# Kernel optimization log

Measured on AMD Instinct MI355X. Metric: run time of the kernel, lower is better.

The kernel has to match this reference:

```python
import jax, jax.numpy as jnp
import numpy as np

B, N, F_IN, F_OUT = 64, 1024, 200, 200
NEG_SLOPE = 0.2  # PyG GATConv default


def setup_inputs() -> dict:
    key = jax.random.key(0)
    k1, k2, k3, k4, k5 = jax.random.split(key, 5)
    return {
        "x": jax.random.normal(k1, (B, 1, N, F_IN), dtype=jnp.float32),
        "W": jax.random.normal(k2, (F_IN, F_OUT), dtype=jnp.float32) * 0.05,
        "att_src": jax.random.normal(k3, (F_OUT,), dtype=jnp.float32) * 0.05,
        "att_dst": jax.random.normal(k4, (F_OUT,), dtype=jnp.float32) * 0.05,
        "bias": jax.random.normal(k5, (F_OUT,), dtype=jnp.float32) * 0.05,
    }


def reference(x, W, att_src, att_dst, bias):
    # x: [B, 1, N, F_IN]; module flattens to (B*N) nodes but the edge_index
    # only spans node ids 0..N-1 (complete graph minus self loops). PyG's
    # GATConv re-adds self loops for ALL B*N nodes, so:
    #   nodes 0..N-1 : dense softmax attention over all N nodes (incl. self)
    #   nodes >= N   : only the self loop -> out = h_i + bias
    b, _, n, f = x.shape
    xf = x.reshape(b * n, f)
    h = xf @ W                                # [B*N, F_OUT] linear transform

    h0 = h[:n]                                # first graph's nodes
    a_s = h0 @ att_src                        # [N] per-source score
    a_d = h0 @ att_dst                        # [N] per-target score
    # score[i, j] = leaky_relu(a_dst[i] + a_src[j]), softmax over sources j
    scores = jax.nn.leaky_relu(a_d[:, None] + a_s[None, :], negative_slope=NEG_SLOPE)
    alpha = jax.nn.softmax(scores, axis=1)    # [N, N]
    out0 = alpha @ h0 + bias                  # [N, F_OUT]

    out_rest = h[n:] + bias                   # self-loop only -> alpha == 1
    out = jnp.concatenate([out0, out_rest], axis=0)
    return out.reshape(b, n, -1)[:, None]     # [B, 1, N, F_OUT]
```

## Files before the change

kernel.cpp:

```cpp
#include <hip/hip_runtime.h>

#define BATCH 64
#define NNODE 1024
#define FDIM  200
#define MROWS (BATCH * NNODE)
#define NEG_SLOPE 0.2f

#define NKT 7
#define NNT 13

typedef short s16x8 __attribute__((ext_vector_type(8)));
typedef float f32x4 __attribute__((ext_vector_type(4)));


__device__ __forceinline__ unsigned int f2bf(float f) {
    unsigned int u = __float_as_uint(f);
    return (u + 0x7fffu + ((u >> 16) & 1u)) >> 16;
}
__device__ __forceinline__ unsigned int pack2(float a, float b) {
    return f2bf(a) | (f2bf(b) << 16);
}

__global__ __launch_bounds__(64) void k_prep(const float* __restrict__ W,
                                             const float* __restrict__ att_src,
                                             const float* __restrict__ att_dst,
                                             unsigned short* __restrict__ fragW,
                                             float* __restrict__ wsv,
                                             float* __restrict__ wdv)
{
    const int b    = blockIdx.x;
    const int lane = threadIdx.x;

    if (b < 91) {
        const int kt   = b / NNT;
        const int nt   = b - kt * NNT;
        const int n    = nt * 16 + (lane & 15);
        const int kb   = kt * 32 + (lane >> 4) * 8;
        s16x8 v;
        #pragma unroll
        for (int j = 0; j < 8; ++j) {
            int k = kb + j;
            float f = (k < FDIM && n < FDIM) ? W[k * FDIM + n] : 0.f;
            v[j] = (short)f2bf(f);
        }
        ((s16x8*)(fragW + (size_t)b * 512))[lane] = v;
    } else {
        const int kk = b - 91;
        const float* Wr = W + kk * FDIM;
        float ps = 0.f, pd = 0.f;
        #pragma unroll
        for (int i = 0; i < 4; ++i) {
            int n = lane + i * 64;
            if (n < FDIM) {
                float wv = Wr[n];
                ps = fmaf(wv, att_src[n], ps);
                pd = fmaf(wv, att_dst[n], pd);
            }
        }
        #pragma unroll
        for (int off = 32; off; off >>= 1) {
            ps += __shfl_down(ps, off);
            pd += __shfl_down(pd, off);
        }
        if (lane == 0) { wsv[kk] = ps; wdv[kk] = pd; }
    }
}

__global__ __launch_bounds__(256) void k_av(const float* __restrict__ x,
                                            const float* __restrict__ wsv,
                                            const float* __restrict__ wdv,
                                            float* __restrict__ a_s,
                                            float* __restrict__ a_d)
{
    const int tid  = threadIdx.x;
    const int lane = tid & 63;
    const int row  = blockIdx.x * 4 + (tid >> 6);
    const float* xr = x + (size_t)row * FDIM;
    float ss = 0.f, sd = 0.f;
    for (int k = lane; k < FDIM; k += 64) {
        float xv = xr[k];
        ss = fmaf(xv, wsv[k], ss);
        sd = fmaf(xv, wdv[k], sd);
    }
    #pragma unroll
    for (int off = 32; off; off >>= 1) {
        ss += __shfl_down(ss, off);
        sd += __shfl_down(sd, off);
    }
    if (lane == 0) { a_s[row] = ss; a_d[row] = sd; }
}

__global__ __launch_bounds__(64) void k_gemm(const float* __restrict__ x,
                                             const unsigned short* __restrict__ fragW,
                                             const float* __restrict__ bias,
                                             float* __restrict__ out,
                                             unsigned short* __restrict__ h0frag)
{
    __shared__ float scr[16][17];
    const int lane = threadIdx.x;
    const int ln   = lane & 15;
    const int quad = lane >> 4;
    const int R0   = blockIdx.x * 16;

    f32x4 acc[NNT];
    #pragma unroll
    for (int nt = 0; nt < NNT; ++nt) acc[nt] = (f32x4){0.f, 0.f, 0.f, 0.f};

    const float* xrow = x + (size_t)(R0 + ln) * FDIM;

    float4 ar[NKT][2];
    #pragma unroll
    for (int kt = 0; kt < 4; ++kt) {
        const float4* ap = (const float4*)(xrow + kt * 32 + quad * 8);
        ar[kt][0] = ap[0]; ar[kt][1] = ap[1];
    }

    s16x8 bc[NNT], bn[NNT];
    #pragma unroll
    for (int nt = 0; nt < NNT; ++nt)
        bc[nt] = *(const s16x8*)(fragW + ((size_t)nt * 64 + lane) * 8);

    #pragma unroll
    for (int kt = 0; kt < NKT; ++kt) {
        if (kt < NKT - 1) {
            #pragma unroll
            for (int nt = 0; nt < NNT; ++nt)
                bn[nt] = *(const s16x8*)(fragW +
                    ((size_t)((kt + 1) * NNT + nt) * 64 + lane) * 8);
        }
        if (kt + 4 < NKT) {
            int ka = kt + 4;
            if (ka < 6) {
                const float4* ap = (const float4*)(xrow + ka * 32 + quad * 8);
                ar[ka][0] = ap[0]; ar[ka][1] = ap[1];
            } else {
                if (quad == 0) {
                    const float4* ap = (const float4*)(xrow + ka * 32);
                    ar[ka][0] = ap[0]; ar[ka][1] = ap[1];
                } else {
                    ar[ka][0] = make_float4(0.f, 0.f, 0.f, 0.f);
                    ar[ka][1] = make_float4(0.f, 0.f, 0.f, 0.f);
                }
            }
        }
        float4 f0 = ar[kt][0], f1 = ar[kt][1];
        unsigned int au[4] = {pack2(f0.x, f0.y), pack2(f0.z, f0.w),
                              pack2(f1.x, f1.y), pack2(f1.z, f1.w)};
        s16x8 a = *(s16x8*)au;
        #pragma unroll
        for (int nt = 0; nt < NNT; ++nt)
            acc[nt] = __builtin_amdgcn_mfma_f32_16x16x32_bf16(a, bc[nt], acc[nt], 0, 0, 0);
        if (kt < NKT - 1) {
            #pragma unroll
            for (int nt = 0; nt < NNT; ++nt) bc[nt] = bn[nt];
        }
    }

    if (R0 >= NNODE) {
        #pragma unroll
        for (int nt = 0; nt < NNT; ++nt) {
            int col = nt * 16 + ln;
            if (nt < 12 || ln < 8) {
                float bv = bias[col];
                #pragma unroll
                for (int r = 0; r < 4; ++r)
                    out[(size_t)(R0 + quad * 4 + r) * FDIM + col] = acc[nt][r] + bv;
            }
        }
    } else {
        const int kt2 = R0 >> 5;
        const int lo  = (R0 >> 4) & 1;
        for (int nt = 0; nt < NNT; ++nt) {
            #pragma unroll
            for (int r = 0; r < 4; ++r) scr[quad * 4 + r][ln] = acc[nt][r];
            __syncthreads();
            if (lane < 32) {
                int oct = lane >> 4, nl = lane & 15;
                uint4 dv;
                dv.x = pack2(scr[oct * 8 + 0][nl], scr[oct * 8 + 1][nl]);
                dv.y = pack2(scr[oct * 8 + 2][nl], scr[oct * 8 + 3][nl]);
                dv.z = pack2(scr[oct * 8 + 4][nl], scr[oct * 8 + 5][nl]);
                dv.w = pack2(scr[oct * 8 + 6][nl], scr[oct * 8 + 7][nl]);
                *(uint4*)(h0frag + ((size_t)(kt2 * NNT + nt) * 64 + lo * 32 + lane) * 8) = dv;
            }
            __syncthreads();
        }
    }
}

__global__ __launch_bounds__(256) void k_stats(const float* __restrict__ a_s,
                                               const float* __restrict__ a_d,
                                               float* __restrict__ m_out,
                                               float* __restrict__ l_out)
{
    __shared__ float as_s[1024];
    const int tid = threadIdx.x;
    #pragma unroll
    for (int i = 0; i < 4; ++i) as_s[tid + i * 256] = a_s[tid + i * 256];
    __syncthreads();

    const int lane = tid & 63;
    const int row  = blockIdx.x * 4 + (tid >> 6);

    float mx = -1e30f;
    #pragma unroll
    for (int i = 0; i < 16; ++i) mx = fmaxf(mx, as_s[lane + i * 64]);
    #pragma unroll
    for (int off = 32; off; off >>= 1) mx = fmaxf(mx, __shfl_down(mx, off));
    mx = __shfl(mx, 0);

    const float ad = a_d[row];
    float mi = ad + mx; mi = (mi > 0.f) ? mi : NEG_SLOPE * mi;

    float sum = 0.f;
    #pragma unroll
    for (int i = 0; i < 16; ++i) {
        float s = ad + as_s[lane + i * 64];
        s = (s > 0.f) ? s : NEG_SLOPE * s;
        sum += __expf(s - mi);
    }
    #pragma unroll
    for (int off = 32; off; off >>= 1) sum += __shfl_down(sum, off);
    if (lane == 0) { m_out[row] = mi; l_out[row] = sum; }
}

__global__ __launch_bounds__(256) void k_attn(const unsigned short* __restrict__ h0frag,
                                              const float* __restrict__ a_s,
                                              const float* __restrict__ a_d,
                                              const float* __restrict__ m_v,
                                              const float* __restrict__ l_v,
                                              const float* __restrict__ bias,
                                              float* __restrict__ out)
{
    const int tid  = threadIdx.x;
    const int lane = tid & 63;
    const int w    = __builtin_amdgcn_readfirstlane(tid >> 6);
    const int ln   = lane & 15;
    const int quad = lane >> 4;
    const int it   = blockIdx.x / NNT;
    const int nt   = blockIdx.x - it * NNT;
    const int i0   = it * 64 + w * 16;

    const float ad = a_d[i0 + ln];
    const float mi = m_v[i0 + ln];

    f32x4 accA = (f32x4){0.f, 0.f, 0.f, 0.f};
    f32x4 accB = (f32x4){0.f, 0.f, 0.f, 0.f};

    #pragma unroll
    for (int kt2 = 0; kt2 < 32; ++kt2) {
        const float4* ap = (const float4*)(a_s + kt2 * 32 + quad * 8);
        float4 f0 = ap[0], f1 = ap[1];
        float e[8] = {f0.x, f0.y, f0.z, f0.w, f1.x, f1.y, f1.z, f1.w};
        #pragma unroll
        for (int j = 0; j < 8; ++j) {
            float s = ad + e[j];
            s = (s > 0.f) ? s : NEG_SLOPE * s;
            e[j] = __expf(s - mi);
        }
        unsigned int au[4] = {pack2(e[0], e[1]), pack2(e[2], e[3]),
                              pack2(e[4], e[5]), pack2(e[6], e[7])};
        s16x8 afrag = *(s16x8*)au;
        s16x8 b = *(const s16x8*)(h0frag + ((size_t)(kt2 * NNT + nt) * 64 + lane) * 8);
        if (kt2 & 1) accB = __builtin_amdgcn_mfma_f32_16x16x32_bf16(afrag, b, accB, 0, 0, 0);
        else         accA = __builtin_amdgcn_mfma_f32_16x16x32_bf16(afrag, b, accA, 0, 0, 0);
    }

    const int col = nt * 16 + ln;
    if (nt < 12 || ln < 8) {
        float bv = bias[col];
        #pragma unroll
        for (int r = 0; r < 4; ++r) {
            float rl = 1.0f / l_v[i0 + quad * 4 + r];
            out[(size_t)(i0 + quad * 4 + r) * FDIM + col]
                = (accA[r] + accB[r]) * rl + bv;
        }
    }
}

extern "C" void kernel_launch(void* const* d_in, const int* in_sizes, int n_in,
                              void* d_out, int out_size, void* d_ws, size_t ws_size,
                              hipStream_t stream)
{
    const float* x       = (const float*)d_in[0];
    const float* W       = (const float*)d_in[1];
    const float* att_src = (const float*)d_in[2];
    const float* att_dst = (const float*)d_in[3];
    const float* bias    = (const float*)d_in[4];
    float* out = (float*)d_out;
    char*  wsb = (char*)d_ws;

    unsigned short* h0frag = (unsigned short*)(wsb + 0);
    float* a_s   = (float*)(wsb + 425984);
    float* a_d   = (float*)(wsb + 430080);
    float* m_i   = (float*)(wsb + 434176);
    float* l_i   = (float*)(wsb + 438272);
    unsigned short* fragW = (unsigned short*)(wsb + 442368);
    float* wsv   = (float*)(wsb + 535552);
    float* wdv   = (float*)(wsb + 536352);

    k_prep <<<291,        64, 0, stream>>>(W, att_src, att_dst, fragW, wsv, wdv);
    k_av   <<<NNODE / 4, 256, 0, stream>>>(x, wsv, wdv, a_s, a_d);
    k_stats<<<NNODE / 4, 256, 0, stream>>>(a_s, a_d, m_i, l_i);
    k_gemm <<<MROWS / 16, 64, 0, stream>>>(x, fragW, bias, out, h0frag);
    k_attn <<<16 * NNT,  256, 0, stream>>>(h0frag, a_s, a_d, m_i, l_i, bias, out);
}
```

Measured before the change: 140.7 us.

## Stage W fragments in LDS for GEMM and split-K attention with reduction

The projection GEMM now runs 256-thread blocks of four waves, each wave handling 32 rows, with the bf16 W fragments loaded cooperatively into LDS in two phases so they are shared across waves instead of each 64-thread block reading them from global memory. The attention kernel changes from one column tile per block to one 16-row tile per block covering all 13 column tiles. The K dimension is split across the four waves and their partial results are reduced through shared memory, and the 1/l normalisation is folded into the probabilities before bf16 packing. The aim is better operand reuse and fewer, larger blocks. The cost is more LDS, extra barriers, only 64 attention blocks, and first-graph rows being written to out before attention overwrites them.

```diff
diff --git a/kernel.cpp b/kernel.cpp
--- a/kernel.cpp
+++ b/kernel.cpp
@@ -32,10 +32,10 @@
     const int lane = threadIdx.x;
 
     if (b < 91) {
-        const int kt   = b / NNT;
-        const int nt   = b - kt * NNT;
-        const int n    = nt * 16 + (lane & 15);
-        const int kb   = kt * 32 + (lane >> 4) * 8;
+        const int kt = b / NNT;
+        const int nt = b - kt * NNT;
+        const int n  = nt * 16 + (lane & 15);
+        const int kb = kt * 32 + (lane >> 4) * 8;
         s16x8 v;
         #pragma unroll
         for (int j = 0; j < 8; ++j) {
@@ -90,104 +90,6 @@
     if (lane == 0) { a_s[row] = ss; a_d[row] = sd; }
 }
 
-__global__ __launch_bounds__(64) void k_gemm(const float* __restrict__ x,
-                                             const unsigned short* __restrict__ fragW,
-                                             const float* __restrict__ bias,
-                                             float* __restrict__ out,
-                                             unsigned short* __restrict__ h0frag)
-{
-    __shared__ float scr[16][17];
-    const int lane = threadIdx.x;
-    const int ln   = lane & 15;
-    const int quad = lane >> 4;
-    const int R0   = blockIdx.x * 16;
-
-    f32x4 acc[NNT];
-    #pragma unroll
-    for (int nt = 0; nt < NNT; ++nt) acc[nt] = (f32x4){0.f, 0.f, 0.f, 0.f};
-
-    const float* xrow = x + (size_t)(R0 + ln) * FDIM;
-
-    float4 ar[NKT][2];
-    #pragma unroll
-    for (int kt = 0; kt < 4; ++kt) {
-        const float4* ap = (const float4*)(xrow + kt * 32 + quad * 8);
-        ar[kt][0] = ap[0]; ar[kt][1] = ap[1];
-    }
-
-    s16x8 bc[NNT], bn[NNT];
-    #pragma unroll
-    for (int nt = 0; nt < NNT; ++nt)
-        bc[nt] = *(const s16x8*)(fragW + ((size_t)nt * 64 + lane) * 8);
-
-    #pragma unroll
-    for (int kt = 0; kt < NKT; ++kt) {
-        if (kt < NKT - 1) {
-            #pragma unroll
-            for (int nt = 0; nt < NNT; ++nt)
-                bn[nt] = *(const s16x8*)(fragW +
-                    ((size_t)((kt + 1) * NNT + nt) * 64 + lane) * 8);
-        }
-        if (kt + 4 < NKT) {
-            int ka = kt + 4;
-            if (ka < 6) {
-                const float4* ap = (const float4*)(xrow + ka * 32 + quad * 8);
-                ar[ka][0] = ap[0]; ar[ka][1] = ap[1];
-            } else {
-                if (quad == 0) {
-                    const float4* ap = (const float4*)(xrow + ka * 32);
-                    ar[ka][0] = ap[0]; ar[ka][1] = ap[1];
-                } else {
-                    ar[ka][0] = make_float4(0.f, 0.f, 0.f, 0.f);
-                    ar[ka][1] = make_float4(0.f, 0.f, 0.f, 0.f);
-                }
-            }
-        }
-        float4 f0 = ar[kt][0], f1 = ar[kt][1];
-        unsigned int au[4] = {pack2(f0.x, f0.y), pack2(f0.z, f0.w),
-                              pack2(f1.x, f1.y), pack2(f1.z, f1.w)};
-        s16x8 a = *(s16x8*)au;
-        #pragma unroll
-        for (int nt = 0; nt < NNT; ++nt)
-            acc[nt] = __builtin_amdgcn_mfma_f32_16x16x32_bf16(a, bc[nt], acc[nt], 0, 0, 0);
-        if (kt < NKT - 1) {
-            #pragma unroll
-            for (int nt = 0; nt < NNT; ++nt) bc[nt] = bn[nt];
-        }
-    }
-
-    if (R0 >= NNODE) {
-        #pragma unroll
-        for (int nt = 0; nt < NNT; ++nt) {
-            int col = nt * 16 + ln;
-            if (nt < 12 || ln < 8) {
-                float bv = bias[col];
-                #pragma unroll
-                for (int r = 0; r < 4; ++r)
-                    out[(size_t)(R0 + quad * 4 + r) * FDIM + col] = acc[nt][r] + bv;
-            }
-        }
-    } else {
-        const int kt2 = R0 >> 5;
-        const int lo  = (R0 >> 4) & 1;
-        for (int nt = 0; nt < NNT; ++nt) {
-            #pragma unroll
-            for (int r = 0; r < 4; ++r) scr[quad * 4 + r][ln] = acc[nt][r];
-            __syncthreads();
-            if (lane < 32) {
-                int oct = lane >> 4, nl = lane & 15;
-                uint4 dv;
-                dv.x = pack2(scr[oct * 8 + 0][nl], scr[oct * 8 + 1][nl]);
-                dv.y = pack2(scr[oct * 8 + 2][nl], scr[oct * 8 + 3][nl]);
-                dv.z = pack2(scr[oct * 8 + 4][nl], scr[oct * 8 + 5][nl]);
-                dv.w = pack2(scr[oct * 8 + 6][nl], scr[oct * 8 + 7][nl]);
-                *(uint4*)(h0frag + ((size_t)(kt2 * NNT + nt) * 64 + lo * 32 + lane) * 8) = dv;
-            }
-            __syncthreads();
-        }
-    }
-}
-
 __global__ __launch_bounds__(256) void k_stats(const float* __restrict__ a_s,
                                                const float* __restrict__ a_d,
                                                float* __restrict__ m_out,
@@ -222,6 +124,129 @@
     #pragma unroll
     for (int off = 32; off; off >>= 1) sum += __shfl_down(sum, off);
     if (lane == 0) { m_out[row] = mi; l_out[row] = sum; }
+}
+
+__global__ __launch_bounds__(256) void k_gemm(const float* __restrict__ x,
+                                              const uint4* __restrict__ fragWg,
+                                              const float* __restrict__ bias,
+                                              float* __restrict__ out,
+                                              unsigned short* __restrict__ h0frag)
+{
+    __shared__ uint4 ldsW4[52 * 64];
+    __shared__ float scr[4][16][17];
+    unsigned short* ldsW = (unsigned short*)ldsW4;
+    const int tid  = threadIdx.x;
+    const int lane = tid & 63;
+    const int w    = __builtin_amdgcn_readfirstlane(tid >> 6);
+    const int ln   = lane & 15;
+    const int quad = lane >> 4;
+    const int R0   = blockIdx.x * 128 + w * 32;
+
+    f32x4 acc[2][NNT];
+    #pragma unroll
+    for (int s = 0; s < 2; ++s)
+        #pragma unroll
+        for (int nt = 0; nt < NNT; ++nt) acc[s][nt] = (f32x4){0.f, 0.f, 0.f, 0.f};
+
+    #pragma unroll
+    for (int i = 0; i < 13; ++i)
+        ldsW4[tid + i * 256] = fragWg[tid + i * 256];
+    __syncthreads();
+
+    #pragma unroll
+    for (int kt = 0; kt < 4; ++kt) {
+        s16x8 a[2];
+        #pragma unroll
+        for (int s = 0; s < 2; ++s) {
+            const float4* ap = (const float4*)(x +
+                (size_t)(R0 + s * 16 + ln) * FDIM + kt * 32 + quad * 8);
+            float4 f0 = ap[0], f1 = ap[1];
+            unsigned int au[4] = {pack2(f0.x, f0.y), pack2(f0.z, f0.w),
+                                  pack2(f1.x, f1.y), pack2(f1.z, f1.w)};
+            a[s] = *(s16x8*)au;
+        }
+        #pragma unroll
+        for (int nt = 0; nt < NNT; ++nt) {
+            s16x8 bf = *(const s16x8*)(ldsW + (kt * NNT + nt) * 512 + lane * 8);
+            #pragma unroll
+            for (int s = 0; s < 2; ++s)
+                acc[s][nt] = __builtin_amdgcn_mfma_f32_16x16x32_bf16(
+                    a[s], bf, acc[s][nt], 0, 0, 0);
+        }
+    }
+
+    __syncthreads();
+    #pragma unroll
+    for (int i = 0; i < 10; ++i) {
+        int idx = tid + i * 256;
+        if (idx < 2496) ldsW4[idx] = fragWg[3328 + idx];
+    }
+    __syncthreads();
+
+    #pragma unroll
+    for (int kt = 4; kt < NKT; ++kt) {
+        s16x8 a[2];
+        #pragma unroll
+        for (int s = 0; s < 2; ++s) {
+            if (kt < 6 || quad == 0) {
+                const float4* ap = (const float4*)(x +
+                    (size_t)(R0 + s * 16 + ln) * FDIM + kt * 32 + quad * 8);
+                float4 f0 = ap[0], f1 = ap[1];
+                unsigned int au[4] = {pack2(f0.x, f0.y), pack2(f0.z, f0.w),
+                                      pack2(f1.x, f1.y), pack2(f1.z, f1.w)};
+                a[s] = *(s16x8*)au;
+            } else {
+                a[s] = (s16x8){0, 0, 0, 0, 0, 0, 0, 0};
+            }
+        }
+        #pragma unroll
+        for (int nt = 0; nt < NNT; ++nt) {
+            s16x8 bf = *(const s16x8*)(ldsW + ((kt - 4) * NNT + nt) * 512 + lane * 8);
+            #pragma unroll
+            for (int s = 0; s < 2; ++s)
+                acc[s][nt] = __builtin_amdgcn_mfma_f32_16x16x32_bf16(
+                    a[s], bf, acc[s][nt], 0, 0, 0);
+        }
+    }
+
+    #pragma unroll
+    for (int nt = 0; nt < NNT; ++nt) {
+        int col = nt * 16 + ln;
+        if (nt < 12 || ln < 8) {
+            float bv = bias[col];
+            #pragma unroll
+            for (int s = 0; s < 2; ++s)
+                #pragma unroll
+                for (int r = 0; r < 4; ++r)
+                    out[(size_t)(R0 + s * 16 + quad * 4 + r) * FDIM + col]
+                        = acc[s][nt][r] + bv;
+        }
+    }
+
+    if (blockIdx.x < 8) {
+        #pragma unroll
+        for (int s = 0; s < 2; ++s) {
+            const int Rg  = R0 + s * 16;
+            const int kt2 = Rg >> 5;
+            const int lo  = (Rg >> 4) & 1;
+            for (int nt = 0; nt < NNT; ++nt) {
+                #pragma unroll
+                for (int r = 0; r < 4; ++r) scr[w][quad * 4 + r][ln] = acc[s][nt][r];
+                __syncthreads();
+                if (lane < 32) {
+                    int oct = lane >> 4, nl = lane & 15;
+                    uint4 dv;
+                    dv.x = pack2(scr[w][oct * 8 + 0][nl], scr[w][oct * 8 + 1][nl]);
+                    dv.y = pack2(scr[w][oct * 8 + 2][nl], scr[w][oct * 8 + 3][nl]);
+                    dv.z = pack2(scr[w][oct * 8 + 4][nl], scr[w][oct * 8 + 5][nl]);
+                    dv.w = pack2(scr[w][oct * 8 + 6][nl], scr[w][oct * 8 + 7][nl]);
+                    *(uint4*)(h0frag +
+                        ((size_t)(kt2 * NNT + nt) * 64 + lo * 32 + lane) * 8) = dv;
+                }
+                __syncthreads();
+            }
+        }
+    }
 }
 
 __global__ __launch_bounds__(256) void k_attn(const unsigned short* __restrict__ h0frag,
@@ -232,48 +257,59 @@
                                               const float* __restrict__ bias,
                                               float* __restrict__ out)
 {
+    __shared__ f32x4 red[4][64][NNT];
     const int tid  = threadIdx.x;
     const int lane = tid & 63;
     const int w    = __builtin_amdgcn_readfirstlane(tid >> 6);
     const int ln   = lane & 15;
     const int quad = lane >> 4;
-    const int it   = blockIdx.x / NNT;
-    const int nt   = blockIdx.x - it * NNT;
-    const int i0   = it * 64 + w * 16;
+    const int i0   = blockIdx.x * 16;
 
     const float ad = a_d[i0 + ln];
     const float mi = m_v[i0 + ln];
-
-    f32x4 accA = (f32x4){0.f, 0.f, 0.f, 0.f};
-    f32x4 accB = (f32x4){0.f, 0.f, 0.f, 0.f};
-
-    #pragma unroll
-    for (int kt2 = 0; kt2 < 32; ++kt2) {
+    const float rl = 1.0f / l_v[i0 + ln];
+
+    f32x4 acc[NNT];
+    #pragma unroll
+    for (int nt = 0; nt < NNT; ++nt) acc[nt] = (f32x4){0.f, 0.f, 0.f, 0.f};
+
+    #pragma unroll
+    for (int kk = 0; kk < 8; ++kk) {
+        const int kt2 = w * 8 + kk;
         const float4* ap = (const float4*)(a_s + kt2 * 32 + quad * 8);
         float4 f0 = ap[0], f1 = ap[1];
         float e[8] = {f0.x, f0.y, f0.z, f0.w, f1.x, f1.y, f1.z, f1.w};
         #pragma unroll
-        for (int j = 0; j < 8; ++j) {
-            float s = ad + e[j];
+        for (int jj = 0; jj < 8; ++jj) {
+            float s = ad + e[jj];
             s = (s > 0.f) ? s : NEG_SLOPE * s;
-            e[j] = __expf(s - mi);
+            e[jj] = __expf(s - mi) * rl;
         }
         unsigned int au[4] = {pack2(e[0], e[1]), pack2(e[2], e[3]),
                               pack2(e[4], e[5]), pack2(e[6], e[7])};
         s16x8 afrag = *(s16x8*)au;
-        s16x8 b = *(const s16x8*)(h0frag + ((size_t)(kt2 * NNT + nt) * 64 + lane) * 8);
-        if (kt2 & 1) accB = __builtin_amdgcn_mfma_f32_16x16x32_bf16(afrag, b, accB, 0, 0, 0);
-        else         accA = __builtin_amdgcn_mfma_f32_16x16x32_bf16(afrag, b, accA, 0, 0, 0);
-    }
-
-    const int col = nt * 16 + ln;
-    if (nt < 12 || ln < 8) {
-        float bv = bias[col];
-        #pragma unroll
-        for (int r = 0; r < 4; ++r) {
-            float rl = 1.0f / l_v[i0 + quad * 4 + r];
-            out[(size_t)(i0 + quad * 4 + r) * FDIM + col]
-                = (accA[r] + accB[r]) * rl + bv;
+        #pragma unroll
+        for (int nt = 0; nt < NNT; ++nt) {
+            s16x8 bf = *(const s16x8*)(h0frag +
+                ((size_t)(kt2 * NNT + nt) * 64 + lane) * 8);
+            acc[nt] = __builtin_amdgcn_mfma_f32_16x16x32_bf16(afrag, bf, acc[nt], 0, 0, 0);
+        }
+    }
+
+    #pragma unroll
+    for (int nt = 0; nt < NNT; ++nt) red[w][lane][nt] = acc[nt];
+    __syncthreads();
+
+    for (int nt = w; nt < NNT; nt += 4) {
+        f32x4 v = red[0][lane][nt];
+        #pragma unroll
+        for (int p = 1; p < 4; ++p) v += red[p][lane][nt];
+        const int col = nt * 16 + ln;
+        if (col < FDIM) {
+            float bv = bias[col];
+            #pragma unroll
+            for (int r = 0; r < 4; ++r)
+                out[(size_t)(i0 + quad * 4 + r) * FDIM + col] = v[r] + bv;
         }
     }
 }
@@ -291,17 +327,17 @@
     char*  wsb = (char*)d_ws;
 
     unsigned short* h0frag = (unsigned short*)(wsb + 0);
-    float* a_s   = (float*)(wsb + 425984);
-    float* a_d   = (float*)(wsb + 430080);
-    float* m_i   = (float*)(wsb + 434176);
-    float* l_i   = (float*)(wsb + 438272);
-    unsigned short* fragW = (unsigned short*)(wsb + 442368);
-    float* wsv   = (float*)(wsb + 535552);
-    float* wdv   = (float*)(wsb + 536352);
-
-    k_prep <<<291,        64, 0, stream>>>(W, att_src, att_dst, fragW, wsv, wdv);
-    k_av   <<<NNODE / 4, 256, 0, stream>>>(x, wsv, wdv, a_s, a_d);
-    k_stats<<<NNODE / 4, 256, 0, stream>>>(a_s, a_d, m_i, l_i);
-    k_gemm <<<MROWS / 16, 64, 0, stream>>>(x, fragW, bias, out, h0frag);
-    k_attn <<<16 * NNT,  256, 0, stream>>>(h0frag, a_s, a_d, m_i, l_i, bias, out);
-}
+    float* a_s = (float*)(wsb + 425984);
+    float* a_d = (float*)(wsb + 430080);
+    float* m_i = (float*)(wsb + 434176);
+    float* l_i = (float*)(wsb + 438272);
+    float* wsv = (float*)(wsb + 442368);
+    float* wdv = (float*)(wsb + 443168);
+    unsigned short* fragW = (unsigned short*)(wsb + 444416);
+
+    k_prep <<<291,         64, 0, stream>>>(W, att_src, att_dst, fragW, wsv, wdv);
+    k_av   <<<NNODE / 4,  256, 0, stream>>>(x, wsv, wdv, a_s, a_d);
+    k_stats<<<NNODE / 4,  256, 0, stream>>>(a_s, a_d, m_i, l_i);
+    k_gemm <<<MROWS / 128, 256, 0, stream>>>(x, (const uint4*)fragW, bias, out, h0frag);
+    k_attn <<<64,         256, 0, stream>>>(h0frag, a_s, a_d, m_i, l_i, bias, out);
+}
```

New measurement: 142.4 us. About the same (+1.2%).
